# Kernel tuning notes

Hardware: AMD Instinct MI355X
Metric: run time of the kernel (lower is better)

The kernel has to match this reference:

```python
import jax, jax.numpy as jnp
import numpy as np

D_MODEL = 512
N_HEADS = 8
POI_N, POI_F = 1683, 24


def _linear_params(k, fan_in, fan_out):
    kw, kb = jax.random.split(k)
    bound = 1.0 / np.sqrt(fan_in)
    w = jax.random.uniform(kw, (fan_in, fan_out), jnp.float32, -bound, bound)
    b = jax.random.uniform(kb, (fan_out,), jnp.float32, -bound, bound)
    return w, b


def setup_inputs() -> dict:
    key = jax.random.key(0)
    ks = jax.random.split(key, 7)
    B, L, D = 8, 8192, D_MODEL
    x = jax.random.normal(ks[0], (B, L, D), jnp.float32)
    poi_data = jax.random.normal(ks[1], (POI_N, POI_F), jnp.float32)
    wq1, bq1 = _linear_params(ks[2], POI_F, 1)
    wq2, bq2 = _linear_params(ks[3], POI_N, D)
    wk, bk = _linear_params(ks[4], D, D)
    wv, bv = _linear_params(ks[5], D, D)
    wo, bo = _linear_params(ks[6], D, D)
    return dict(x=x, poi_data=poi_data, wq1=wq1, bq1=bq1, wq2=wq2, bq2=bq2,
                wk=wk, bk=bk, wv=wv, bv=bv, wo=wo, bo=bo)


def reference(x, poi_data, wq1, bq1, wq2, bq2, wk, bk, wv, bv, wo, bo):
    B, L, D = x.shape
    H = N_HEADS
    d = D // H
    # key / value projections: [B, L, H, d]
    k = (x @ wk + bk).reshape(B, L, H, d)
    v = (x @ wv + bv).reshape(B, L, H, d)
    # query: Linear(24,1) over poi features, squeeze, Linear(1683, d_model)
    q = (poi_data @ wq1 + bq1)[:, 0]          # [1683]
    q = (q @ wq2 + bq2).reshape(H, d)         # [H, d] -- shared across B and L
    scale = 1.0 / jnp.sqrt(jnp.asarray(d, x.dtype))
    # Original computes scores [B,H,L,L] where every row l is identical
    # (query is broadcast over L). Mathematically equivalent collapsed form:
    scores = jnp.einsum('he,bshe->bhs', q, k)  # [B, H, L]
    A = jax.nn.softmax(scale * scores, axis=-1)
    V = jnp.einsum('bhs,bshd->bhd', A, v).reshape(B, H * d)  # [B, D]
    out = jnp.broadcast_to(V[:, None, :], (B, L, H * d))      # same row for all L
    return out @ wo + bo
```

## Files before the change

### kernel.cpp

```cpp
#include <hip/hip_runtime.h>
#include <math.h>

#define L_SEQ 8192
#define B_N   8

typedef float f4v __attribute__((ext_vector_type(4)));

#define QKV_OFF    0
#define V_OFF      4096
#define ROW_OFF    8192
#define QFP_OFF    12288
#define DPART_OFF  40960
#define YPART_OFF  65536

__global__ __launch_bounds__(512) void k2_qf(const float* __restrict__ poi,
                                             const float* __restrict__ wq1,
                                             const float* __restrict__ bq1,
                                             const float* __restrict__ wq2, float* ws) {
    __shared__ float qr[32];
    int k = blockIdx.x, t = threadIdx.x;
    int i0 = k * 32;
    int cnt = 1683 - i0; if (cnt > 32) cnt = 32;
    if (t < cnt) {
        float a = bq1[0];
#pragma unroll
        for (int j = 0; j < 24; ++j) a += poi[(i0 + t) * 24 + j] * wq1[j];
        qr[t] = a;
    }
    __syncthreads();
    float a = 0.f;
    for (int ii = 0; ii < cnt; ++ii) a += qr[ii] * wq2[(size_t)(i0 + ii) * 512 + t];
    ws[QFP_OFF + k * 512 + t] = a;
}

__global__ void k3_qkvec(const float* __restrict__ wk, const float* __restrict__ bq2,
                         const float* __restrict__ bv, const float* __restrict__ bo, float* ws) {
    __shared__ float qf[512];
    int t = threadIdx.x, bid = blockIdx.x;
    for (int o = t; o < 512; o += 256) {
        float s = bq2[o];
        for (int k = 0; k < 53; ++k) s += ws[QFP_OFF + k * 512 + o];
        qf[o] = s;
    }
    __syncthreads();
    int idx = bid * 256 + t;
    int h = idx >> 9, c = idx & 511;
    float a = 0.f;
#pragma unroll 8
    for (int e = 0; e < 64; ++e) a += qf[h * 64 + e] * wk[(size_t)c * 512 + h * 64 + e];
    ws[QKV_OFF + idx] = 0.125f * a;
    if (bid < 8) {
        ws[V_OFF + bid * 512 + t]       = bv[t];
        ws[V_OFF + bid * 512 + 256 + t] = bv[256 + t];
    } else {
        int b = bid - 8;
        ws[ROW_OFF + b * 512 + t]       = bo[t];
        ws[ROW_OFF + b * 512 + 256 + t] = bo[256 + t];
    }
}

__global__ __launch_bounds__(256, 2) void kF(const float* __restrict__ x, float* __restrict__ ws) {
    __shared__ float num_s[4096];
    __shared__ float den_s[8];
    int t = threadIdx.x;
    int lane = t & 63, w = t >> 6;
    int b = blockIdx.x >> 6, slot = blockIdx.x & 63;
    int wslot = slot * 4 + w;

    float4 qa[8], qb[8];
    {
        const float4* qg4 = (const float4*)(ws + QKV_OFF);
#pragma unroll
        for (int h = 0; h < 8; ++h) {
            qa[h] = qg4[h * 128 + lane * 2];
            qb[h] = qg4[h * 128 + lane * 2 + 1];
        }
    }

    const int b0 = lane & 1, b1 = (lane >> 1) & 1, b2 = (lane >> 2) & 1;
    float num[8][8] = {{0.f}};
    float den_own = 0.f;

    const float4* xp = (const float4*)(x + (size_t)b * L_SEQ * 512);

    for (int r = wslot; r < L_SEQ; r += 512) {
        int r2 = r + 256;
        float4 xa1 = xp[(size_t)r  * 128 + lane * 2];
        float4 xb1 = xp[(size_t)r  * 128 + lane * 2 + 1];
        float4 xa2 = xp[(size_t)r2 * 128 + lane * 2];
        float4 xb2 = xp[(size_t)r2 * 128 + lane * 2 + 1];

        float p1[8], p2[8];
#pragma unroll
        for (int h = 0; h < 8; ++h) {
            p1[h] = xa1.x * qa[h].x + xa1.y * qa[h].y + xa1.z * qa[h].z + xa1.w * qa[h].w
                  + xb1.x * qb[h].x + xb1.y * qb[h].y + xb1.z * qb[h].z + xb1.w * qb[h].w;
            p2[h] = xa2.x * qa[h].x + xa2.y * qa[h].y + xa2.z * qa[h].z + xa2.w * qa[h].w
                  + xb2.x * qb[h].x + xb2.y * qb[h].y + xb2.z * qb[h].z + xb2.w * qb[h].w;
        }
        float sA, sB;
        {
            float a0 = b0 ? p1[1] : p1[0], t0 = b0 ? p1[0] : p1[1];
            float a1 = b0 ? p1[3] : p1[2], t1 = b0 ? p1[2] : p1[3];
            float a2 = b0 ? p1[5] : p1[4], t2 = b0 ? p1[4] : p1[5];
            float a3 = b0 ? p1[7] : p1[6], t3 = b0 ? p1[6] : p1[7];
            float c0 = b0 ? p2[1] : p2[0], u0 = b0 ? p2[0] : p2[1];
            float c1 = b0 ? p2[3] : p2[2], u1 = b0 ? p2[2] : p2[3];
            float c2 = b0 ? p2[5] : p2[4], u2 = b0 ? p2[4] : p2[5];
            float c3 = b0 ? p2[7] : p2[6], u3 = b0 ? p2[6] : p2[7];
            float vA0 = a0 + __shfl_xor(t0, 1, 64);
            float vA1 = a1 + __shfl_xor(t1, 1, 64);
            float vA2 = a2 + __shfl_xor(t2, 1, 64);
            float vA3 = a3 + __shfl_xor(t3, 1, 64);
            float vB0 = c0 + __shfl_xor(u0, 1, 64);
            float vB1 = c1 + __shfl_xor(u1, 1, 64);
            float vB2 = c2 + __shfl_xor(u2, 1, 64);
            float vB3 = c3 + __shfl_xor(u3, 1, 64);
            float wA0 = b1 ? vA1 : vA0, sA0 = b1 ? vA0 : vA1;
            float wA1 = b1 ? vA3 : vA2, sA1 = b1 ? vA2 : vA3;
            float wB0 = b1 ? vB1 : vB0, sB0 = b1 ? vB0 : vB1;
            float wB1 = b1 ? vB3 : vB2, sB1 = b1 ? vB2 : vB3;
            float uA0 = wA0 + __shfl_xor(sA0, 2, 64);
            float uA1 = wA1 + __shfl_xor(sA1, 2, 64);
            float uB0 = wB0 + __shfl_xor(sB0, 2, 64);
            float uB1 = wB1 + __shfl_xor(sB1, 2, 64);
            float zA = b2 ? uA1 : uA0, yA = b2 ? uA0 : uA1;
            float zB = b2 ? uB1 : uB0, yB = b2 ? uB0 : uB1;
            sA = zA + __shfl_xor(yA, 4, 64);
            sB = zB + __shfl_xor(yB, 4, 64);
        }
        sA += __shfl_xor(sA, 8, 64);  sB += __shfl_xor(sB, 8, 64);
        sA += __shfl_xor(sA, 16, 64); sB += __shfl_xor(sB, 16, 64);
        sA += __shfl_xor(sA, 32, 64); sB += __shfl_xor(sB, 32, 64);
        float wgA = __expf(sA), wgB = __expf(sB);
        den_own += wgA + wgB;
        float wa[8], wb[8];
#pragma unroll
        for (int h = 0; h < 8; ++h) { wa[h] = __shfl(wgA, h, 64); wb[h] = __shfl(wgB, h, 64); }
#pragma unroll
        for (int h = 0; h < 8; ++h) {
            num[h][0] += wa[h] * xa1.x + wb[h] * xa2.x;
            num[h][1] += wa[h] * xa1.y + wb[h] * xa2.y;
            num[h][2] += wa[h] * xa1.z + wb[h] * xa2.z;
            num[h][3] += wa[h] * xa1.w + wb[h] * xa2.w;
            num[h][4] += wa[h] * xb1.x + wb[h] * xb2.x;
            num[h][5] += wa[h] * xb1.y + wb[h] * xb2.y;
            num[h][6] += wa[h] * xb1.z + wb[h] * xb2.z;
            num[h][7] += wa[h] * xb1.w + wb[h] * xb2.w;
        }
    }

    for (int wi = 0; wi < 4; ++wi) {
        if (w == wi) {
#pragma unroll
            for (int h = 0; h < 8; ++h) {
                int base = h * 512 + lane * 8;
                if (wi == 0) {
#pragma unroll
                    for (int j = 0; j < 8; ++j) num_s[base + j] = num[h][j];
                } else {
#pragma unroll
                    for (int j = 0; j < 8; ++j) num_s[base + j] += num[h][j];
                }
            }
            if (lane < 8) { if (wi == 0) den_s[lane] = den_own; else den_s[lane] += den_own; }
        }
        __syncthreads();
    }
    float4* yp4 = (float4*)(ws + YPART_OFF + (size_t)blockIdx.x * 4096);
    const float4* ns4 = (const float4*)num_s;
#pragma unroll
    for (int k = 0; k < 4; ++k) yp4[k * 256 + t] = ns4[k * 256 + t];
    if (t < 8) ws[DPART_OFF + blockIdx.x * 8 + t] = den_s[t];
}

__global__ __launch_bounds__(512) void kV(const float* __restrict__ wv, float* ws) {
    __shared__ float red[512];
    __shared__ float yn_s[512];
    __shared__ float dinv[8];
    int b = blockIdx.x >> 3, cc = blockIdx.x & 7;
    int c0 = cc * 64;
    int t = threadIdx.x;
    red[t] = ws[DPART_OFF + (size_t)(b * 64 + (t >> 3)) * 8 + (t & 7)];
    __syncthreads();
#pragma unroll
    for (int off = 256; off >= 8; off >>= 1) {
        if (t < off) red[t] += red[t + off];
        __syncthreads();
    }
    if (t < 8) dinv[t] = 1.f / red[t];
    int h = t >> 6, cl = t & 63;
    float s = 0.f;
    const float* yp = ws + YPART_OFF + (size_t)(b * 64) * 4096 + h * 512 + c0 + cl;
#pragma unroll 8
    for (int sl = 0; sl < 64; ++sl) s += yp[(size_t)sl * 4096];
    __syncthreads();
    yn_s[t] = s * dinv[h];
    __syncthreads();
    int o = t, ho = o >> 6;
    const float* yh = yn_s + ho * 64;
    float acc = 0.f;
#pragma unroll 8
    for (int ci = 0; ci < 64; ++ci) acc += yh[ci] * wv[(size_t)(c0 + ci) * 512 + o];
    atomicAdd(ws + V_OFF + b * 512 + o, acc);
}

__global__ __launch_bounds__(512) void kRow(const float* __restrict__ wo, float* ws) {
    __shared__ float V_s[64];
    int b = blockIdx.x >> 3, oc = blockIdx.x & 7;
    int o0 = oc * 64;
    int t = threadIdx.x;
    if (t < 64) V_s[t] = ws[V_OFF + b * 512 + o0 + t];
    __syncthreads();
    float acc = 0.f;
#pragma unroll 8
    for (int oi = 0; oi < 64; ++oi) acc += V_s[oi] * wo[(size_t)(o0 + oi) * 512 + t];
    atomicAdd(ws + ROW_OFF + b * 512 + t, acc);
}

__global__ __launch_bounds__(256) void k9_out(const float* __restrict__ ws, float* __restrict__ out) {
    const f4v* row4 = (const f4v*)(ws + ROW_OFF);
    f4v* out4 = (f4v*)out;
    size_t stride = (size_t)gridDim.x * blockDim.x;
    for (size_t g = (size_t)blockIdx.x * blockDim.x + threadIdx.x; g < 8388608ull; g += stride) {
        int b = (int)(g >> 20);
        int q = (int)(g & 127);
        f4v v = row4[b * 128 + q];
        __builtin_nontemporal_store(v, &out4[g]);
    }
}

extern "C" void kernel_launch(void* const* d_in, const int* in_sizes, int n_in,
                              void* d_out, int out_size, void* d_ws, size_t ws_size,
                              hipStream_t stream) {
    const float* x   = (const float*)d_in[0];
    const float* poi = (const float*)d_in[1];
    const float* wq1 = (const float*)d_in[2];
    const float* bq1 = (const float*)d_in[3];
    const float* wq2 = (const float*)d_in[4];
    const float* bq2 = (const float*)d_in[5];
    const float* wk  = (const float*)d_in[6];
    const float* bk  = (const float*)d_in[7];
    const float* wv  = (const float*)d_in[8];
    const float* bv  = (const float*)d_in[9];
    const float* wo  = (const float*)d_in[10];
    const float* bo  = (const float*)d_in[11];
    float* ws  = (float*)d_ws;
    float* out = (float*)d_out;
    (void)bk;

    k2_qf<<<53, 512, 0, stream>>>(poi, wq1, bq1, wq2, ws);
    k3_qkvec<<<16, 256, 0, stream>>>(wk, bq2, bv, bo, ws);
    kF<<<512, 256, 0, stream>>>(x, ws);
    kV<<<64, 512, 0, stream>>>(wv, ws);
    kRow<<<64, 512, 0, stream>>>(wo, ws);
    k9_out<<<2048, 256, 0, stream>>>(ws, out);
}
```

Before: 89.80 us.

## Use DPP/swizzle lane reductions in kF and fuse V and output projections

Result: faster. 84.66 us (-5.7%).

```diff
diff --git a/kernel.cpp b/kernel.cpp
--- a/kernel.cpp
+++ b/kernel.cpp
@@ -7,11 +7,15 @@
 typedef float f4v __attribute__((ext_vector_type(4)));
 
 #define QKV_OFF    0
-#define V_OFF      4096
 #define ROW_OFF    8192
 #define QFP_OFF    12288
 #define DPART_OFF  40960
 #define YPART_OFF  65536
+
+#define DPPADD(keep, send, CTRL) \
+    ((keep) + __int_as_float(__builtin_amdgcn_update_dpp(0, __float_as_int(send), (CTRL), 0xF, 0xF, true)))
+#define SWZADD(v, PAT) ((v) + __int_as_float(__builtin_amdgcn_ds_swizzle(__float_as_int(v), (PAT))))
+#define SWZ(v, PAT)    (__int_as_float(__builtin_amdgcn_ds_swizzle(__float_as_int(v), (PAT))))
 
 __global__ __launch_bounds__(512) void k2_qf(const float* __restrict__ poi,
                                              const float* __restrict__ wq1,
@@ -34,7 +38,7 @@
 }
 
 __global__ void k3_qkvec(const float* __restrict__ wk, const float* __restrict__ bq2,
-                         const float* __restrict__ bv, const float* __restrict__ bo, float* ws) {
+                         const float* __restrict__ bo, float* ws) {
     __shared__ float qf[512];
     int t = threadIdx.x, bid = blockIdx.x;
     for (int o = t; o < 512; o += 256) {
@@ -49,10 +53,7 @@
 #pragma unroll 8
     for (int e = 0; e < 64; ++e) a += qf[h * 64 + e] * wk[(size_t)c * 512 + h * 64 + e];
     ws[QKV_OFF + idx] = 0.125f * a;
-    if (bid < 8) {
-        ws[V_OFF + bid * 512 + t]       = bv[t];
-        ws[V_OFF + bid * 512 + 256 + t] = bv[256 + t];
-    } else {
+    if (bid >= 8) {
         int b = bid - 8;
         ws[ROW_OFF + b * 512 + t]       = bo[t];
         ws[ROW_OFF + b * 512 + 256 + t] = bo[256 + t];
@@ -77,7 +78,7 @@
         }
     }
 
-    const int b0 = lane & 1, b1 = (lane >> 1) & 1, b2 = (lane >> 2) & 1;
+    const int b0 = lane & 1, b1 = (lane >> 1) & 1, b3 = (lane >> 3) & 1;
     float num[8][8] = {{0.f}};
     float den_own = 0.f;
 
@@ -98,45 +99,35 @@
             p2[h] = xa2.x * qa[h].x + xa2.y * qa[h].y + xa2.z * qa[h].z + xa2.w * qa[h].w
                   + xb2.x * qb[h].x + xb2.y * qb[h].y + xb2.z * qb[h].z + xb2.w * qb[h].w;
         }
-        float sA, sB;
-        {
-            float a0 = b0 ? p1[1] : p1[0], t0 = b0 ? p1[0] : p1[1];
-            float a1 = b0 ? p1[3] : p1[2], t1 = b0 ? p1[2] : p1[3];
-            float a2 = b0 ? p1[5] : p1[4], t2 = b0 ? p1[4] : p1[5];
-            float a3 = b0 ? p1[7] : p1[6], t3 = b0 ? p1[6] : p1[7];
-            float c0 = b0 ? p2[1] : p2[0], u0 = b0 ? p2[0] : p2[1];
-            float c1 = b0 ? p2[3] : p2[2], u1 = b0 ? p2[2] : p2[3];
-            float c2 = b0 ? p2[5] : p2[4], u2 = b0 ? p2[4] : p2[5];
-            float c3 = b0 ? p2[7] : p2[6], u3 = b0 ? p2[6] : p2[7];
-            float vA0 = a0 + __shfl_xor(t0, 1, 64);
-            float vA1 = a1 + __shfl_xor(t1, 1, 64);
-            float vA2 = a2 + __shfl_xor(t2, 1, 64);
-            float vA3 = a3 + __shfl_xor(t3, 1, 64);
-            float vB0 = c0 + __shfl_xor(u0, 1, 64);
-            float vB1 = c1 + __shfl_xor(u1, 1, 64);
-            float vB2 = c2 + __shfl_xor(u2, 1, 64);
-            float vB3 = c3 + __shfl_xor(u3, 1, 64);
-            float wA0 = b1 ? vA1 : vA0, sA0 = b1 ? vA0 : vA1;
-            float wA1 = b1 ? vA3 : vA2, sA1 = b1 ? vA2 : vA3;
-            float wB0 = b1 ? vB1 : vB0, sB0 = b1 ? vB0 : vB1;
-            float wB1 = b1 ? vB3 : vB2, sB1 = b1 ? vB2 : vB3;
-            float uA0 = wA0 + __shfl_xor(sA0, 2, 64);
-            float uA1 = wA1 + __shfl_xor(sA1, 2, 64);
-            float uB0 = wB0 + __shfl_xor(sB0, 2, 64);
-            float uB1 = wB1 + __shfl_xor(sB1, 2, 64);
-            float zA = b2 ? uA1 : uA0, yA = b2 ? uA0 : uA1;
-            float zB = b2 ? uB1 : uB0, yB = b2 ? uB0 : uB1;
-            sA = zA + __shfl_xor(yA, 4, 64);
-            sB = zB + __shfl_xor(yB, 4, 64);
-        }
-        sA += __shfl_xor(sA, 8, 64);  sB += __shfl_xor(sB, 8, 64);
-        sA += __shfl_xor(sA, 16, 64); sB += __shfl_xor(sB, 16, 64);
-        sA += __shfl_xor(sA, 32, 64); sB += __shfl_xor(sB, 32, 64);
+
+        float vA0 = DPPADD(b0 ? p1[1] : p1[0], b0 ? p1[0] : p1[1], 0xB1);
+        float vA1 = DPPADD(b0 ? p1[3] : p1[2], b0 ? p1[2] : p1[3], 0xB1);
+        float vA2 = DPPADD(b0 ? p1[5] : p1[4], b0 ? p1[4] : p1[5], 0xB1);
+        float vA3 = DPPADD(b0 ? p1[7] : p1[6], b0 ? p1[6] : p1[7], 0xB1);
+        float vB0 = DPPADD(b0 ? p2[1] : p2[0], b0 ? p2[0] : p2[1], 0xB1);
+        float vB1 = DPPADD(b0 ? p2[3] : p2[2], b0 ? p2[2] : p2[3], 0xB1);
+        float vB2 = DPPADD(b0 ? p2[5] : p2[4], b0 ? p2[4] : p2[5], 0xB1);
+        float vB3 = DPPADD(b0 ? p2[7] : p2[6], b0 ? p2[6] : p2[7], 0xB1);
+        float uA0 = DPPADD(b1 ? vA1 : vA0, b1 ? vA0 : vA1, 0x4E);
+        float uA1 = DPPADD(b1 ? vA3 : vA2, b1 ? vA2 : vA3, 0x4E);
+        float uB0 = DPPADD(b1 ? vB1 : vB0, b1 ? vB0 : vB1, 0x4E);
+        float uB1 = DPPADD(b1 ? vB3 : vB2, b1 ? vB2 : vB3, 0x4E);
+        float sA = DPPADD(b3 ? uA1 : uA0, b3 ? uA0 : uA1, 0x128);
+        float sB = DPPADD(b3 ? uB1 : uB0, b3 ? uB0 : uB1, 0x128);
+        sA = SWZADD(sA, 0x101F);  sB = SWZADD(sB, 0x101F);
+        sA = SWZADD(sA, 0x401F);  sB = SWZADD(sB, 0x401F);
+        sA += __shfl_xor(sA, 32, 64);
+        sB += __shfl_xor(sB, 32, 64);
+
         float wgA = __expf(sA), wgB = __expf(sB);
         den_own += wgA + wgB;
+
         float wa[8], wb[8];
-#pragma unroll
-        for (int h = 0; h < 8; ++h) { wa[h] = __shfl(wgA, h, 64); wb[h] = __shfl(wgB, h, 64); }
+        wa[0] = SWZ(wgA,   0); wa[1] = SWZ(wgA,  32); wa[2] = SWZ(wgA,  64); wa[3] = SWZ(wgA,  96);
+        wa[4] = SWZ(wgA, 256); wa[5] = SWZ(wgA, 288); wa[6] = SWZ(wgA, 320); wa[7] = SWZ(wgA, 352);
+        wb[0] = SWZ(wgB,   0); wb[1] = SWZ(wgB,  32); wb[2] = SWZ(wgB,  64); wb[3] = SWZ(wgB,  96);
+        wb[4] = SWZ(wgB, 256); wb[5] = SWZ(wgB, 288); wb[6] = SWZ(wgB, 320); wb[7] = SWZ(wgB, 352);
+
 #pragma unroll
         for (int h = 0; h < 8; ++h) {
             num[h][0] += wa[h] * xa1.x + wb[h] * xa2.x;
@@ -163,7 +154,10 @@
                     for (int j = 0; j < 8; ++j) num_s[base + j] += num[h][j];
                 }
             }
-            if (lane < 8) { if (wi == 0) den_s[lane] = den_own; else den_s[lane] += den_own; }
+            if ((lane & 52) == 0) {
+                int hh = (lane & 3) | ((lane & 8) >> 1);
+                if (wi == 0) den_s[hh] = den_own; else den_s[hh] += den_own;
+            }
         }
         __syncthreads();
     }
@@ -174,48 +168,54 @@
     if (t < 8) ws[DPART_OFF + blockIdx.x * 8 + t] = den_s[t];
 }
 
-__global__ __launch_bounds__(512) void kV(const float* __restrict__ wv, float* ws) {
+__global__ __launch_bounds__(512) void kVR(const float* __restrict__ wv,
+                                           const float* __restrict__ bv,
+                                           const float* __restrict__ wo, float* ws) {
     __shared__ float red[512];
     __shared__ float yn_s[512];
-    __shared__ float dinv[8];
-    int b = blockIdx.x >> 3, cc = blockIdx.x & 7;
-    int c0 = cc * 64;
+    __shared__ float V_s[64];
+    int b = blockIdx.x >> 3, h = blockIdx.x & 7;
     int t = threadIdx.x;
-    red[t] = ws[DPART_OFF + (size_t)(b * 64 + (t >> 3)) * 8 + (t & 7)];
-    __syncthreads();
-#pragma unroll
-    for (int off = 256; off >= 8; off >>= 1) {
+    red[t] = (t < 64) ? ws[DPART_OFF + (size_t)(b * 64 + t) * 8 + h] : 0.f;
+    __syncthreads();
+#pragma unroll
+    for (int off = 32; off >= 1; off >>= 1) {
         if (t < off) red[t] += red[t + off];
         __syncthreads();
     }
-    if (t < 8) dinv[t] = 1.f / red[t];
-    int h = t >> 6, cl = t & 63;
-    float s = 0.f;
-    const float* yp = ws + YPART_OFF + (size_t)(b * 64) * 4096 + h * 512 + c0 + cl;
-#pragma unroll 8
-    for (int sl = 0; sl < 64; ++sl) s += yp[(size_t)sl * 4096];
-    __syncthreads();
-    yn_s[t] = s * dinv[h];
-    __syncthreads();
-    int o = t, ho = o >> 6;
-    const float* yh = yn_s + ho * 64;
-    float acc = 0.f;
-#pragma unroll 8
-    for (int ci = 0; ci < 64; ++ci) acc += yh[ci] * wv[(size_t)(c0 + ci) * 512 + o];
-    atomicAdd(ws + V_OFF + b * 512 + o, acc);
-}
-
-__global__ __launch_bounds__(512) void kRow(const float* __restrict__ wo, float* ws) {
-    __shared__ float V_s[64];
-    int b = blockIdx.x >> 3, oc = blockIdx.x & 7;
-    int o0 = oc * 64;
-    int t = threadIdx.x;
-    if (t < 64) V_s[t] = ws[V_OFF + b * 512 + o0 + t];
-    __syncthreads();
-    float acc = 0.f;
-#pragma unroll 8
-    for (int oi = 0; oi < 64; ++oi) acc += V_s[oi] * wo[(size_t)(o0 + oi) * 512 + t];
-    atomicAdd(ws + ROW_OFF + b * 512 + t, acc);
+    float dinv = 1.f / red[0];
+    __syncthreads();
+    {
+        float s = 0.f;
+        const float* yp = ws + YPART_OFF + (size_t)(b * 64) * 4096 + h * 512 + t;
+#pragma unroll 8
+        for (int sl = 0; sl < 64; ++sl) s += yp[(size_t)sl * 4096];
+        yn_s[t] = s * dinv;
+    }
+    __syncthreads();
+    {
+        int ol = t & 63, sl = t >> 6;
+        float acc = 0.f;
+        const float* yb = yn_s + sl * 64;
+        const float* wvp = wv + (size_t)(sl * 64) * 512 + h * 64 + ol;
+#pragma unroll 8
+        for (int ci = 0; ci < 64; ++ci) acc += yb[ci] * wvp[(size_t)ci * 512];
+        red[t] = acc;
+    }
+    __syncthreads();
+    if (t < 64) {
+        float acc = bv[h * 64 + t];
+#pragma unroll
+        for (int sl = 0; sl < 8; ++sl) acc += red[sl * 64 + t];
+        V_s[t] = acc;
+    }
+    __syncthreads();
+    {
+        float acc = 0.f;
+#pragma unroll 8
+        for (int oi = 0; oi < 64; ++oi) acc += V_s[oi] * wo[(size_t)(h * 64 + oi) * 512 + t];
+        atomicAdd(ws + ROW_OFF + b * 512 + t, acc);
+    }
 }
 
 __global__ __launch_bounds__(256) void k9_out(const float* __restrict__ ws, float* __restrict__ out) {
@@ -250,9 +250,8 @@
     (void)bk;
 
     k2_qf<<<53, 512, 0, stream>>>(poi, wq1, bq1, wq2, ws);
-    k3_qkvec<<<16, 256, 0, stream>>>(wk, bq2, bv, bo, ws);
+    k3_qkvec<<<16, 256, 0, stream>>>(wk, bq2, bo, ws);
     kF<<<512, 256, 0, stream>>>(x, ws);
-    kV<<<64, 512, 0, stream>>>(wv, ws);
-    kRow<<<64, 512, 0, stream>>>(wo, ws);
+    kVR<<<64, 512, 0, stream>>>(wv, bv, wo, ws);
     k9_out<<<2048, 256, 0, stream>>>(ws, out);
 }
```
